# Optimization experiments

Measured on AMD Instinct MI355X. Metric: run time of the kernel, lower is better.

The kernel has to match this reference:

```python
import jax, jax.numpy as jnp
import numpy as np

NUM_GROUP, GROUP_SIZE = 128, 32
MASK = (64, 32, 32)
FEAT_DIM, N_POINTS = 1024, 2048
NBR_K = int(1.2 * GROUP_SIZE)  # int(nbr_ratio * group_size) = 38
SUPPORT, NBHD = 8, 32
W_RECON, W_MATCH, W_LATENT, W_MAN = 1.0, 1.0, 1.0, 0.1

gather = jax.vmap(lambda p, i: p[i])  # batched index_points

def sqdist(a, b):  # [B,M,3],[B,N,3] -> [B,M,N]
    return (jnp.sum(a * a, -1)[:, :, None] + jnp.sum(b * b, -1)[:, None, :]
            - 2.0 * jnp.einsum('bmd,bnd->bmn', a, b))

def knn_idx(q, db, k):  # indices into db of k nearest to each query
    return jax.lax.top_k(-sqdist(q, db), k)[1]

def fps(pts, G):  # farthest point sampling, [B,N,3] -> [B,G] indices
    b, n, _ = pts.shape
    def step(carry, _):
        min_d, far = carry
        cur = jnp.take_along_axis(pts, far[:, None, None], axis=1)
        min_d = jnp.minimum(min_d, jnp.sum((pts - cur) ** 2, -1))
        return (min_d, jnp.argmax(min_d, -1).astype(jnp.int32)), far
    init = (jnp.full((b, n), 1e10, dtype=pts.dtype), jnp.zeros((b,), jnp.int32))
    _, idxs = jax.lax.scan(step, init, None, length=G)
    return idxs.T

def bn(h, g, b_, m, v):  # BatchNorm1d, eval-mode running stats
    return (h - m) * jax.lax.rsqrt(v + 1e-5) * g + b_

def chamfer_l1(a, b):
    d = sqdist(a, b)
    d1 = jnp.sqrt(jnp.maximum(jnp.min(d, axis=2), 1e-12))
    d2 = jnp.sqrt(jnp.maximum(jnp.min(d, axis=1), 1e-12))
    return 0.5 * (d1.mean() + d2.mean())

def estimate_normals(xyz, K):  # PCA normal per point + direction disambiguation
    nb = gather(xyz, knn_idx(xyz, xyz, K))          # [B,N,K,3]
    c = nb - nb.mean(axis=2, keepdims=True)
    cov = jnp.einsum('bnki,bnkj->bnij', c, c) / K   # [B,N,3,3]
    _, v = jnp.linalg.eigh(cov)
    n = v[..., 0]                                   # smallest-eigenvalue eigvec
    proj = jnp.einsum('bnkd,bnd->bn', nb - xyz[:, :, None, :], n)
    return n * jnp.where(proj >= 0.0, 1.0, -1.0)[..., None]

def forward_all(pts, W1, b1, g1, be1, m1, v1, W2, b2, W3, b3, g2, be2, m2, v2,
                W4, b4, D1W, D1b, D2W, D2b, D3W, D3b, D4W, D4b):
    bsz = pts.shape[0]
    def encoder(x):  # PCN encoder: pointwise convs + global max pooling
        n = x.shape[1]
        h = jax.nn.relu(bn(x @ W1.T + b1, g1, be1, m1, v1))
        h = h @ W2.T + b2                           # [B,n,256]
        gmax = h.max(axis=1)
        h = jnp.concatenate([jnp.broadcast_to(gmax[:, None, :], (bsz, n, gmax.shape[-1])), h], axis=-1)
        h = jax.nn.relu(bn(h @ W3.T + b3, g2, be2, m2, v2))
        return (h @ W4.T + b4).max(axis=1)          # [B,FEAT_DIM]
    def decoder(z):
        h = jax.nn.relu(z @ D1W.T + D1b)
        h = jax.nn.relu(h @ D2W.T + D2b)
        h = jax.nn.relu(h @ D3W.T + D3b)
        return (h @ D4W.T + D4b).reshape(bsz, -1, 3)
    # --- Group divider: FPS centers + knn neighborhoods (centered) ---
    center = gather(pts, fps(pts, NUM_GROUP))       # [B,G,3]
    nbrs = gather(pts, knn_idx(center, pts, GROUP_SIZE)) - center[:, :, None, :]
    o1, o2 = MASK[0], MASK[0] + MASK[1]             # identity perm partition
    ng = (nbrs[:, :o1], nbrs[:, o1:o2], nbrs[:, o2:])
    cg = (center[:, :o1], center[:, o1:o2], center[:, o2:])
    rebuild0 = (ng[0] + cg[0][:, :, None, :]).reshape(bsz, -1, 3)
    feat = encoder(rebuild0)
    pred = decoder(feat)                            # [B,N_POINTS,3]
    # shape reconstruction loss
    idx = knn_idx(cg[0], pred, NBR_K)
    l_recon = W_RECON * chamfer_l1(rebuild0, gather(pred, idx).reshape(bsz, -1, 3))
    # shape matching loss
    rebuild1 = (ng[1] + cg[1][:, :, None, :]).reshape(bsz, -1, 3)
    idx = knn_idx(cg[1], pred, NBR_K)
    l_match = W_MATCH * chamfer_l1(rebuild1, gather(pred, idx).reshape(bsz, -1, 3))
    # latent reconstruction (detached input) - SmoothL1
    idx = knn_idx(cg[2], pred, GROUP_SIZE)
    feat_recon = encoder(jax.lax.stop_gradient(gather(pred, idx).reshape(bsz, -1, 3)))
    diff = feat - feat_recon
    ad = jnp.abs(diff)
    l_latent = W_LATENT * jnp.where(ad < 1.0, 0.5 * diff * diff, ad - 0.5).mean()
    # manifoldness (normal consistency) constraint
    normals = estimate_normals(pred, NBHD)
    nb = gather(normals, knn_idx(pred, pred, SUPPORT))  # [B,N,8,3]
    a = nb[:, :, :1, :]
    cos = jnp.sum(a * nb, -1) / (jnp.maximum(jnp.linalg.norm(a, axis=-1), 1e-6)
                                 * jnp.maximum(jnp.linalg.norm(nb, axis=-1), 1e-6))
    l_man = W_MAN * jnp.std(1.0 - cos, axis=-1, ddof=1).mean(axis=-1).mean()
    total = l_recon + l_match + l_latent + l_man
    return total, l_recon, l_match, l_latent, l_man


def setup_inputs() -> dict:
    ks = jax.random.split(jax.random.key(0), 10)
    rn = lambda k, sh: jax.random.normal(k, sh, jnp.float32) * 0.02
    z, o = jnp.zeros, jnp.ones
    return dict(
        pts=jax.random.normal(ks[0], (16, 2048, 3), jnp.float32),
        W1=rn(ks[1], (128, 3)), b1=z(128), g1=o(128), be1=z(128), m1=z(128), v1=o(128),
        W2=rn(ks[2], (256, 128)), b2=z(256),
        W3=rn(ks[3], (512, 512)), b3=z(512), g2=o(512), be2=z(512), m2=z(512), v2=o(512),
        W4=rn(ks[4], (FEAT_DIM, 512)), b4=z(FEAT_DIM),
        D1W=rn(ks[5], (2048, FEAT_DIM)), D1b=z(2048),
        D2W=rn(ks[6], (2048, 2048)), D2b=z(2048),
        D3W=rn(ks[7], (2048, 2048)), D3b=z(2048),
        D4W=rn(ks[8], (3 * N_POINTS, 2048)), D4b=z(3 * N_POINTS),
    )


def reference(pts, W1, b1, g1, be1, m1, v1, W2, b2, W3, b3, g2, be2, m2, v2,
              W4, b4, D1W, D1b, D2W, D2b, D3W, D3b, D4W, D4b):
    return forward_all(pts, W1, b1, g1, be1, m1, v1, W2, b2, W3, b3, g2, be2,
                       m2, v2, W4, b4, D1W, D1b, D2W, D2b, D3W, D3b, D4W, D4b)
```

## Files before the change

### kernel.cpp

```cpp
#include <hip/hip_runtime.h>
#include <math.h>

#define BSZ 16
#define NPTS 2048
#define NG 128
#define GS 32
#define NBRK 38

typedef _Float16 f16;
typedef _Float16 f16x8 __attribute__((ext_vector_type(8)));
typedef float f32x4 __attribute__((ext_vector_type(4)));

__device__ __forceinline__ unsigned fkey(float x) {
    unsigned u = __float_as_uint(x);
    return (u >> 31) ? ~u : (u | 0x80000000u);
}
__device__ __forceinline__ float fkey_inv(unsigned k) {
    unsigned u = (k >> 31) ? (k ^ 0x80000000u) : ~k;
    return __uint_as_float(u);
}

__device__ __forceinline__ unsigned wave_min_u32(unsigned v) {
    unsigned t;
    t = (unsigned)__builtin_amdgcn_update_dpp(-1, (int)v, 0x111, 0xF, 0xF, false);
    v = v < t ? v : t;
    t = (unsigned)__builtin_amdgcn_update_dpp(-1, (int)v, 0x112, 0xF, 0xF, false);
    v = v < t ? v : t;
    t = (unsigned)__builtin_amdgcn_update_dpp(-1, (int)v, 0x114, 0xF, 0xF, false);
    v = v < t ? v : t;
    t = (unsigned)__builtin_amdgcn_update_dpp(-1, (int)v, 0x118, 0xF, 0xF, false);
    v = v < t ? v : t;
    t = (unsigned)__builtin_amdgcn_update_dpp(-1, (int)v, 0x142, 0xA, 0xF, false);
    v = v < t ? v : t;
    t = (unsigned)__builtin_amdgcn_update_dpp(-1, (int)v, 0x143, 0xC, 0xF, false);
    v = v < t ? v : t;
    return (unsigned)__builtin_amdgcn_readlane((int)v, 63);
}

__device__ __forceinline__ unsigned long long wave_max_u64(unsigned long long v) {
#define DPPSTEP(ctrl, rmask)                                                                \
    {                                                                                       \
        unsigned tlo = (unsigned)__builtin_amdgcn_update_dpp(0, (int)(unsigned)v, ctrl,     \
                                                             rmask, 0xF, false);            \
        unsigned thi = (unsigned)__builtin_amdgcn_update_dpp(0, (int)(unsigned)(v >> 32),   \
                                                             ctrl, rmask, 0xF, false);      \
        unsigned long long t = ((unsigned long long)thi << 32) | tlo;                       \
        v = t > v ? t : v;                                                                  \
    }
    DPPSTEP(0x111, 0xF)
    DPPSTEP(0x112, 0xF)
    DPPSTEP(0x114, 0xF)
    DPPSTEP(0x118, 0xF)
    DPPSTEP(0x142, 0xA)
    DPPSTEP(0x143, 0xC)
#undef DPPSTEP
    unsigned rlo = (unsigned)__builtin_amdgcn_readlane((int)(unsigned)v, 63);
    unsigned rhi = (unsigned)__builtin_amdgcn_readlane((int)(unsigned)(v >> 32), 63);
    return ((unsigned long long)rhi << 32) | rlo;
}

__global__ __launch_bounds__(256, 1) void fps_kernel_v5(const float* __restrict__ pts,
                                                        float* __restrict__ center) {
    int b = blockIdx.x;
    const float* P = pts + (size_t)b * NPTS * 3;
    int tid = threadIdx.x;
    int lane = tid & 63, wave = tid >> 6;
    __shared__ __align__(16) float Pl[NPTS * 3];
    __shared__ __align__(16) float slot[2][4][8];
#pragma unroll
    for (int i = 0; i < 6; ++i) {
        int v4 = tid + i * 256;
        ((f32x4*)Pl)[v4] = ((const f32x4*)P)[v4];
    }
    __syncthreads();
    float px[8], py[8], pz[8], mind[8];
#pragma unroll
    for (int m = 0; m < 8; ++m) {
        int j = tid + (m << 8);
        px[m] = Pl[j * 3 + 0];
        py[m] = Pl[j * 3 + 1];
        pz[m] = Pl[j * 3 + 2];
        mind[m] = 1e10f;
    }
    float cx = Pl[0], cy = Pl[1], cz = Pl[2];
    float* C = center + (size_t)b * NG * 3;
#pragma unroll 1
    for (int g = 0; g < NG; ++g) {
        if (tid == 0) {
            C[g * 3 + 0] = cx; C[g * 3 + 1] = cy; C[g * 3 + 2] = cz;
        }
        if (g == NG - 1) break;
        float best0 = -1.f, best1 = -1.f;
        int bm0 = 0, bm1 = 1;
#pragma unroll
        for (int m = 0; m < 8; m += 2) {
            float dx0 = px[m] - cx, dy0 = py[m] - cy, dz0 = pz[m] - cz;
            float d0 = dx0 * dx0 + dy0 * dy0 + dz0 * dz0;
            float md0 = fminf(mind[m], d0);
            mind[m] = md0;
            if (md0 > best0) { best0 = md0; bm0 = m; }
            float dx1 = px[m + 1] - cx, dy1 = py[m + 1] - cy, dz1 = pz[m + 1] - cz;
            float d1 = dx1 * dx1 + dy1 * dy1 + dz1 * dz1;
            float md1 = fminf(mind[m + 1], d1);
            mind[m + 1] = md1;
            if (md1 > best1) { best1 = md1; bm1 = m + 1; }
        }
        bool t = (best1 > best0) || (best1 == best0 && bm1 < bm0);
        float bv = t ? best1 : best0;
        int bi = t ? bm1 : bm0;
        unsigned j = (unsigned)(tid + (bi << 8));
        unsigned long long key =
            ((unsigned long long)__float_as_uint(bv) << 32) | (unsigned)(~j);
        key = wave_max_u64(key);
        unsigned bj = ~(unsigned)key;
        int par = g & 1;
        if (lane < 3) slot[par][wave][2 + lane] = Pl[bj * 3 + lane];
        if (lane == 0) {
            slot[par][wave][0] = __uint_as_float((unsigned)key);
            slot[par][wave][1] = __uint_as_float((unsigned)(key >> 32));
        }
        __syncthreads();
        unsigned long long kb = 0ull;
        float nx = 0.f, ny = 0.f, nz = 0.f;
#pragma unroll
        for (int w = 0; w < 4; ++w) {
            f32x4 v = *(const f32x4*)&slot[par][w][0];
            float vz = slot[par][w][4];
            unsigned long long kk =
                ((unsigned long long)__float_as_uint(v[1]) << 32) | __float_as_uint(v[0]);
            bool tw = kk > kb;
            kb = tw ? kk : kb;
            nx = tw ? v[2] : nx;
            ny = tw ? v[3] : ny;
            nz = tw ? vz : nz;
        }
        cx = nx; cy = ny; cz = nz;
    }
}

__device__ __forceinline__ void knn_query(const float* __restrict__ q,
                                          const float* __restrict__ db,
                                          int k, int* __restrict__ o, int lane) {
    const unsigned KINF = 0xFFFFFFFFu;
    float qx = q[0], qy = q[1], qz = q[2];
    float qq = qx * qx + qy * qy + qz * qz;
    unsigned key[32];
    unsigned c0 = KINF, c1 = KINF, c2 = KINF, c3 = KINF;
#pragma unroll
    for (int m = 0; m < 32; ++m) {
        int j = lane + (m << 6);
        float bx = db[j * 3 + 0], by = db[j * 3 + 1], bz = db[j * 3 + 2];
        float dv = qq + bx * bx + by * by + bz * bz - 2.0f * (qx * bx + qy * by + qz * bz);
        unsigned qd = (unsigned)fminf(fmaxf(dv, 0.f) * 8192.0f, 2097151.f);
        unsigned kk = (qd << 11) | (unsigned)j;
        key[m] = kk;
        if (kk < c3) {
            if (kk < c2) {
                c3 = c2;
                if (kk < c1) {
                    c2 = c1;
                    if (kk < c0) { c1 = c0; c0 = kk; } else c1 = kk;
                } else c2 = kk;
            } else c3 = kk;
        }
    }
    unsigned hw = c3;
    int ncached = 4;
    for (int r = 0; r < k; ++r) {
        bool need = (c0 == KINF) && (ncached < 32);
        if (__any(need)) {
            unsigned best = KINF;
#pragma unroll
            for (int m = 0; m < 32; ++m) {
                unsigned v = key[m];
                best = (v > hw && v < best) ? v : best;
            }
            if (need) {
                c0 = best;
                hw = best;
                ncached = (best == KINF) ? 32 : ncached + 1;
            }
        }
        unsigned g = wave_min_u32(c0);
        if (lane == 0) o[r] = (int)(g & 0x7FFu);
        if (((g & 0x7FFu) & 63u) == (unsigned)lane) {
            c0 = c1; c1 = c2; c2 = c3; c3 = KINF;
        }
    }
}

__global__ void knn_kernel_v7(const float* __restrict__ Q, int q_bstride, int q_off, int nq,
                              const float* __restrict__ DB, int k,
                              int* __restrict__ out, int nbatch) {
    int wave = threadIdx.x >> 6, lane = threadIdx.x & 63;
    int qidx = blockIdx.x * 4 + wave;
    if (qidx >= nbatch * nq) return;
    int b = qidx / nq, qi = qidx % nq;
    knn_query(Q + ((size_t)b * q_bstride + q_off + qi) * 3,
              DB + (size_t)b * NPTS * 3, k, out + (size_t)qidx * k, lane);
}

__global__ void knn_post_kernel(const float* __restrict__ center,
                                const float* __restrict__ pred,
                                int* __restrict__ idxa, int* __restrict__ idxb,
                                int* __restrict__ idxc, int* __restrict__ knn32) {
    int wave = threadIdx.x >> 6, lane = threadIdx.x & 63;
    if (blockIdx.x < 512) {
        int qidx = blockIdx.x * 4 + wave;
        int b = qidx >> 7, qi = qidx & 127;
        const float* q = center + ((size_t)b * NG + qi) * 3;
        const float* db = pred + (size_t)b * NPTS * 3;
        int k; int* o;
        if (qi < 64) { k = NBRK; o = idxa + ((size_t)b * 64 + qi) * NBRK; }
        else if (qi < 96) { k = NBRK; o = idxb + ((size_t)b * 32 + qi - 64) * NBRK; }
        else { k = GS; o = idxc + ((size_t)b * 32 + qi - 96) * GS; }
        knn_query(q, db, k, o, lane);
    } else {
        int qidx = (blockIdx.x - 512) * 4 + wave;
        int b = qidx >> 11, qi = qidx & 2047;
        const float* db = pred + (size_t)b * NPTS * 3;
        knn_query(db + (size_t)qi * 3, db, GS, knn32 + (size_t)qidx * GS, lane);
    }
}

__global__ void gather_rebuild_kernel(const float* __restrict__ pts,
                                      const int* __restrict__ knnc,
                                      float* __restrict__ rebuild0,
                                      float* __restrict__ rebuild1,
                                      f32x4* __restrict__ r0p4,
                                      f32x4* __restrict__ r1p4) {
    int t = blockIdx.x * 256 + threadIdx.x;
    if (t < BSZ * 2048) {
        int b = t >> 11, j = t & 2047;
        int s = knnc[(size_t)b * (NG * GS) + j];
        const float* p = pts + ((size_t)b * NPTS + s) * 3;
        float x = p[0], y = p[1], z = p[2];
        rebuild0[(size_t)t * 3 + 0] = x;
        rebuild0[(size_t)t * 3 + 1] = y;
        rebuild0[(size_t)t * 3 + 2] = z;
        r0p4[t] = (f32x4){x, y, z, x * x + y * y + z * z};
    } else {
        int tt = t - BSZ * 2048;
        int b = tt >> 10, j = tt & 1023;
        int s = knnc[(size_t)b * (NG * GS) + 2048 + j];
        const float* p = pts + ((size_t)b * NPTS + s) * 3;
        float x = p[0], y = p[1], z = p[2];
        rebuild1[(size_t)tt * 3 + 0] = x;
        rebuild1[(size_t)tt * 3 + 1] = y;
        rebuild1[(size_t)tt * 3 + 2] = z;
        r1p4[tt] = (f32x4){x, y, z, x * x + y * y + z * z};
    }
}

__global__ void gather_abc_kernel(const float* __restrict__ pred,
                                  const int* __restrict__ idxa,
                                  const int* __restrict__ idxb,
                                  const int* __restrict__ idxc,
                                  f32x4* __restrict__ gap4,
                                  f32x4* __restrict__ gbp4,
                                  float* __restrict__ gathc) {
    const int NA = BSZ * 2432, NB_ = BSZ * 1216, NC = BSZ * 1024;
    int t = blockIdx.x * 256 + threadIdx.x;
    if (t < NA) {
        int b = t / 2432, j = t - b * 2432;
        int s = idxa[(size_t)b * 2432 + j];
        const float* p = pred + ((size_t)b * NPTS + s) * 3;
        float x = p[0], y = p[1], z = p[2];
        gap4[t] = (f32x4){x, y, z, x * x + y * y + z * z};
    } else if (t < NA + NB_) {
        int tt = t - NA;
        int b = tt / 1216, j = tt - b * 1216;
        int s = idxb[(size_t)b * 1216 + j];
        const float* p = pred + ((size_t)b * NPTS + s) * 3;
        float x = p[0], y = p[1], z = p[2];
        gbp4[tt] = (f32x4){x, y, z, x * x + y * y + z * z};
    } else if (t < NA + NB_ + NC) {
        int tt = t - NA - NB_;
        int b = tt >> 10, j = tt & 1023;
        int s = idxc[(size_t)b * 1024 + j];
        const float* p = pred + ((size_t)b * NPTS + s) * 3;
        gathc[(size_t)tt * 3 + 0] = p[0];
        gathc[(size_t)tt * 3 + 1] = p[1];
        gathc[(size_t)tt * 3 + 2] = p[2];
    }
}

__global__ void cvt_all_kernel(const float* __restrict__ W2, const float* __restrict__ W3,
                               const float* __restrict__ W4, f16* __restrict__ W2h,
                               f16* __restrict__ W3h, f16* __restrict__ W4h) {
    int t = blockIdx.x * 256 + threadIdx.x;
    if (t < 32768) {
        int n = t >> 7, k = t & 127;
        W2h[t] = (f16)W2[(size_t)n * 128 + k];
    } else if (t < 163840) {
        int u = t - 32768;
        int n = u >> 8, k = u & 255;
        W3h[u] = (f16)W3[(size_t)n * 512 + 256 + k];
    } else if (t < 688128) {
        int u = t - 163840;
        int n = u >> 9, k = u & 511;
        W4h[u] = (f16)W4[(size_t)n * 512 + k];
    }
}

__global__ void layer1_kernel(const float* __restrict__ X, const float* __restrict__ W1,
                              const float* __restrict__ b1, const float* __restrict__ g1,
                              const float* __restrict__ be1, const float* __restrict__ m1,
                              const float* __restrict__ v1, f16* __restrict__ H1, int M) {
    __shared__ float w[384], bb[128], sg[128], sb[128], sm[128], sv[128];
    for (int i = threadIdx.x; i < 384; i += 256) w[i] = W1[i];
    if (threadIdx.x < 128) {
        int c = threadIdx.x;
        bb[c] = b1[c]; sg[c] = g1[c]; sb[c] = be1[c]; sm[c] = m1[c]; sv[c] = v1[c];
    }
    __syncthreads();
    int t = blockIdx.x * 256 + threadIdx.x;
    if (t >= M * 16) return;
    int row = t >> 4, cg = (t & 15) * 8;
    float x0 = X[(size_t)row * 3], x1 = X[(size_t)row * 3 + 1], x2 = X[(size_t)row * 3 + 2];
    f16x8 outv;
#pragma unroll
    for (int j = 0; j < 8; ++j) {
        int c = cg + j;
        float tv = x0 * w[c * 3] + x1 * w[c * 3 + 1] + x2 * w[c * 3 + 2] + bb[c];
        float vv = (tv - sm[c]) * rsqrtf(sv[c] + 1e-5f) * sg[c] + sb[c];
        outv[j] = (f16)fmaxf(vv, 0.f);
    }
    *(f16x8*)&H1[(size_t)row * 128 + cg] = outv;
}

__global__ __launch_bounds__(256) void mfma_gemm_kernel(
        const f16* __restrict__ A, const f16* __restrict__ W, int K, int N,
        const float* __restrict__ bias, const float* __restrict__ bias2d,
        const float* __restrict__ bng, const float* __restrict__ bnb,
        const float* __restrict__ bnm, const float* __restrict__ bnv,
        f16* __restrict__ Cout, unsigned* __restrict__ maxkey,
        int rows_per_batch, int relu) {
    __shared__ f16 Als[128 * 40];
    __shared__ f16 Bls[128 * 40];
    int tid = threadIdx.x;
    int lane = tid & 63;
    int wave = tid >> 6;
    int wm = wave & 1, wn = wave >> 1;
    int c16 = lane & 15, quad = lane >> 4;
    int gx = gridDim.x;
    int nwg = gx * gridDim.y;
    int lin = blockIdx.y * gx + blockIdx.x;
    int qc = nwg >> 3, rc = nwg & 7;
    int xcd = lin & 7, pos = lin >> 3;
    int nlin = (xcd < rc ? xcd * (qc + 1) : rc * (qc + 1) + (xcd - rc) * qc) + pos;
    int row0 = (nlin / gx) * 128, col0 = (nlin % gx) * 128;
    int sr = tid >> 2;
    int skc = (tid & 3) * 8;

    f32x4 acc[4][4];
#pragma unroll
    for (int i = 0; i < 4; ++i)
#pragma unroll
        for (int j = 0; j < 4; ++j) acc[i][j] = (f32x4){0.f, 0.f, 0.f, 0.f};

    const f16* Ab = A + (size_t)(row0 + sr) * K + skc;
    const f16* Ab2 = A + (size_t)(row0 + sr + 64) * K + skc;
    const f16* Wb = W + (size_t)(col0 + sr) * K + skc;
    const f16* Wb2 = W + (size_t)(col0 + sr + 64) * K + skc;

    f16x8 pa0 = *(const f16x8*)Ab;
    f16x8 pa1 = *(const f16x8*)Ab2;
    f16x8 pb0 = *(const f16x8*)Wb;
    f16x8 pb1 = *(const f16x8*)Wb2;

    for (int k0 = 0; k0 < K; k0 += 32) {
        *(f16x8*)&Als[sr * 40 + skc] = pa0;
        *(f16x8*)&Als[(sr + 64) * 40 + skc] = pa1;
        *(f16x8*)&Bls[sr * 40 + skc] = pb0;
        *(f16x8*)&Bls[(sr + 64) * 40 + skc] = pb1;
        __syncthreads();
        if (k0 + 32 < K) {
            int kn = k0 + 32;
            pa0 = *(const f16x8*)(Ab + kn);
            pa1 = *(const f16x8*)(Ab2 + kn);
            pb0 = *(const f16x8*)(Wb + kn);
            pb1 = *(const f16x8*)(Wb2 + kn);
        }
        f16x8 af[4], bf[4];
#pragma unroll
        for (int s = 0; s < 4; ++s) {
            af[s] = *(const f16x8*)&Als[(wm * 64 + s * 16 + c16) * 40 + quad * 8];
            bf[s] = *(const f16x8*)&Bls[(wn * 64 + s * 16 + c16) * 40 + quad * 8];
        }
#pragma unroll
        for (int ms = 0; ms < 4; ++ms)
#pragma unroll
            for (int ns = 0; ns < 4; ++ns)
                acc[ms][ns] = __builtin_amdgcn_mfma_f32_16x16x32_f16(af[ms], bf[ns],
                                                                     acc[ms][ns], 0, 0, 0);
        __syncthreads();
    }

    int b = row0 / rows_per_batch;
#pragma unroll
    for (int ns = 0; ns < 4; ++ns) {
        int col = col0 + wn * 64 + ns * 16 + c16;
        float bv = bias ? bias[col] : 0.f;
        float b2v = bias2d ? bias2d[(size_t)b * N + col] : 0.f;
        float mx = -3e38f;
#pragma unroll
        for (int ms = 0; ms < 4; ++ms) {
#pragma unroll
            for (int j = 0; j < 4; ++j) {
                float v = acc[ms][ns][j] + bv + b2v;
                if (bng) v = (v - bnm[col]) * rsqrtf(bnv[col] + 1e-5f) * bng[col] + bnb[col];
                if (relu) v = fmaxf(v, 0.f);
                if (Cout)
                    Cout[(size_t)(row0 + wm * 64 + ms * 16 + quad * 4 + j) * N + col] = (f16)v;
                mx = fmaxf(mx, v);
            }
        }
        if (maxkey) {
            mx = fmaxf(mx, __shfl_xor(mx, 16, 64));
            mx = fmaxf(mx, __shfl_xor(mx, 32, 64));
            if (quad == 0) atomicMax(&maxkey[(size_t)b * N + col], fkey(mx));
        }
    }
}

__global__ void skinny_v2_kernel(const float* __restrict__ A, const float* __restrict__ W,
                                 int ldw, int woff, const float* __restrict__ bias,
                                 float* __restrict__ C, int K, int N, int relu, int akey) {
    int wave = threadIdx.x >> 6, lane = threadIdx.x & 63;
    int col = blockIdx.x * 4 + wave;
    if (col >= N) return;
    const float* w = W + (size_t)col * ldw + woff;
    float acc[16];
#pragma unroll
    for (int m = 0; m < 16; ++m) acc[m] = 0.f;
    for (int k0 = 0; k0 < K; k0 += 256) {
        f32x4 wv = *(const f32x4*)(w + k0 + lane * 4);
#pragma unroll
        for (int m = 0; m < 16; ++m) {
            f32x4 av = *(const f32x4*)(A + (size_t)m * K + k0 + lane * 4);
            if (akey) {
#pragma unroll
                for (int u = 0; u < 4; ++u) av[u] = fkey_inv(__float_as_uint(av[u]));
            }
            acc[m] += av[0] * wv[0] + av[1] * wv[1] + av[2] * wv[2] + av[3] * wv[3];
        }
    }
#pragma unroll
    for (int m = 0; m < 16; ++m)
#pragma unroll
        for (int s = 1; s < 64; s <<= 1) acc[m] += __shfl_xor(acc[m], s, 64);
    if (lane == 0) {
        float bv = bias[col];
#pragma unroll
        for (int m = 0; m < 16; ++m) {
            float v = acc[m] + bv;
            if (relu) v = fmaxf(v, 0.f);
            C[(size_t)m * N + col] = v;
        }
    }
}

__global__ __launch_bounds__(256) void chamfer4_kernel(const f32x4* __restrict__ r0p4,
                                                       const f32x4* __restrict__ gap4,
                                                       const f32x4* __restrict__ r1p4,
                                                       const f32x4* __restrict__ gbp4,
                                                       float* __restrict__ accum) {
    __shared__ __align__(16) float Bl[2432 * 4];
    int blk = blockIdx.x;
    const f32x4 *A4, *B4; int na, nb, base, bpb; float* slot;
    if (blk < 128)      { A4 = r0p4; na = 2048; B4 = gap4; nb = 2432; slot = accum + 0; base = 0;   bpb = 8; }
    else if (blk < 288) { A4 = gap4; na = 2432; B4 = r0p4; nb = 2048; slot = accum + 1; base = 128; bpb = 10; }
    else if (blk < 352) { A4 = r1p4; na = 1024; B4 = gbp4; nb = 1216; slot = accum + 2; base = 288; bpb = 4; }
    else                { A4 = gbp4; na = 1216; B4 = r1p4; nb = 1024; slot = accum + 3; base = 352; bpb = 5; }
    int rel = blk - base;
    int b = rel / bpb, chunk = rel - b * bpb;
    for (int i = threadIdx.x; i < nb; i += 256)
        ((f32x4*)Bl)[i] = B4[(size_t)b * nb + i];
    __syncthreads();
    int aidx = chunk * 256 + threadIdx.x;
    float val = 0.f;
    if (aidx < na) {
        f32x4 a = A4[(size_t)b * na + aidx];
        float m2x = -2.f * a[0], m2y = -2.f * a[1], m2z = -2.f * a[2];
        float m0 = 3e38f, m1 = 3e38f, m2 = 3e38f, m3 = 3e38f;
        for (int j = 0; j < nb; j += 4) {
            f32x4 b0 = ((const f32x4*)Bl)[j + 0];
            f32x4 b1 = ((const f32x4*)Bl)[j + 1];
            f32x4 b2 = ((const f32x4*)Bl)[j + 2];
            f32x4 b3 = ((const f32x4*)Bl)[j + 3];
            float t0 = fmaf(m2z, b0[2], fmaf(m2y, b0[1], fmaf(m2x, b0[0], b0[3])));
            float t1 = fmaf(m2z, b1[2], fmaf(m2y, b1[1], fmaf(m2x, b1[0], b1[3])));
            float t2 = fmaf(m2z, b2[2], fmaf(m2y, b2[1], fmaf(m2x, b2[0], b2[3])));
            float t3 = fmaf(m2z, b3[2], fmaf(m2y, b3[1], fmaf(m2x, b3[0], b3[3])));
            m0 = fminf(m0, t0); m1 = fminf(m1, t1);
            m2 = fminf(m2, t2); m3 = fminf(m3, t3);
        }
        float m = fminf(fminf(m0, m1), fminf(m2, m3));
        val = sqrtf(fmaxf(a[3] + m, 1e-12f));
    }
    __shared__ float sdata[256];
    sdata[threadIdx.x] = val;
    __syncthreads();
    for (int s = 128; s > 0; s >>= 1) {
        if (threadIdx.x < s) sdata[threadIdx.x] += sdata[threadIdx.x + s];
        __syncthreads();
    }
    if (threadIdx.x == 0) atomicAdd(slot, sdata[0]);
}

__global__ void latent_kernel(const unsigned* __restrict__ k1,
                              const unsigned* __restrict__ k2,
                              int n, float* __restrict__ slot) {
    int t = blockIdx.x * blockDim.x + threadIdx.x;
    float val = 0.f;
    if (t < n) {
        float d = fkey_inv(k1[t]) - fkey_inv(k2[t]);
        float ad = fabsf(d);
        val = (ad < 1.f) ? (0.5f * d * d) : (ad - 0.5f);
    }
    __shared__ float sdata[256];
    sdata[threadIdx.x] = val;
    __syncthreads();
    for (int s = 128; s > 0; s >>= 1) {
        if (threadIdx.x < s) sdata[threadIdx.x] += sdata[threadIdx.x + s];
        __syncthreads();
    }
    if (threadIdx.x == 0) atomicAdd(slot, sdata[0]);
}

__device__ void smallest_evec(double cxx, double cxy, double cxz,
                              double cyy, double cyz, double czz, double ev[3]) {
    double p1 = cxy * cxy + cxz * cxz + cyz * cyz;
    double q = (cxx + cyy + czz) / 3.0;
    double p2 = (cxx - q) * (cxx - q) + (cyy - q) * (cyy - q) + (czz - q) * (czz - q) + 2.0 * p1;
    double lam = q;
    if (p2 > 0.0) {
        double p = sqrt(p2 / 6.0);
        double b00 = (cxx - q) / p, b11 = (cyy - q) / p, b22 = (czz - q) / p;
        double b01 = cxy / p, b02 = cxz / p, b12 = cyz / p;
        double detB = b00 * (b11 * b22 - b12 * b12) - b01 * (b01 * b22 - b12 * b02)
                    + b02 * (b01 * b12 - b11 * b02);
        double r = detB * 0.5;
        r = r < -1.0 ? -1.0 : (r > 1.0 ? 1.0 : r);
        double phi = acos(r) / 3.0;
        lam = q + 2.0 * p * cos(phi + 2.0943951023931953);
    }
    double r0x = cxx - lam, r0y = cxy, r0z = cxz;
    double r1x = cxy, r1y = cyy - lam, r1z = cyz;
    double r2x = cxz, r2y = cyz, r2z = czz - lam;
    double c0x = r0y * r1z - r0z * r1y, c0y = r0z * r1x - r0x * r1z, c0z = r0x * r1y - r0y * r1x;
    double c1x = r0y * r2z - r0z * r2y, c1y = r0z * r2x - r0x * r2z, c1z = r0x * r2y - r0y * r2x;
    double c2x = r1y * r2z - r1z * r2y, c2y = r1z * r2x - r1x * r2z, c2z = r1x * r2y - r1y * r2x;
    double n0 = c0x * c0x + c0y * c0y + c0z * c0z;
    double n1 = c1x * c1x + c1y * c1y + c1z * c1z;
    double n2 = c2x * c2x + c2y * c2y + c2z * c2z;
    double bx = c0x, by = c0y, bz = c0z, bn = n0;
    if (n1 > bn) { bx = c1x; by = c1y; bz = c1z; bn = n1; }
    if (n2 > bn) { bx = c2x; by = c2y; bz = c2z; bn = n2; }
    if (bn < 1e-280) { ev[0] = 1.0; ev[1] = 0.0; ev[2] = 0.0; return; }
    double inv = 1.0 / sqrt(bn);
    ev[0] = bx * inv; ev[1] = by * inv; ev[2] = bz * inv;
}

__global__ __launch_bounds__(64) void normals_kernel(const float* __restrict__ pred,
                                                     const int* __restrict__ knn,
                                                     float* __restrict__ nrm) {
    int t = blockIdx.x * 64 + threadIdx.x;
    if (t >= BSZ * NPTS) return;
    int b = t / NPTS, i = t % NPTS;
    const float* P = pred + (size_t)b * NPTS * 3;
    const int* id = knn + (size_t)t * 32;
    double sx = 0, sy = 0, sz = 0;
    double sxx = 0, sxy = 0, sxz = 0, syy = 0, syz = 0, szz = 0;
#pragma unroll
    for (int k0 = 0; k0 < 32; k0 += 4) {
        int4 jj = *(const int4*)&id[k0];
#pragma unroll
        for (int u = 0; u < 4; ++u) {
            int j = (u == 0) ? jj.x : (u == 1) ? jj.y : (u == 2) ? jj.z : jj.w;
            double x = (double)P[j * 3 + 0];
            double y = (double)P[j * 3 + 1];
            double z = (double)P[j * 3 + 2];
            sx += x; sy += y; sz += z;
            sxx += x * x; sxy += x * y; sxz += x * z;
            syy += y * y; syz += y * z; szz += z * z;
        }
    }
    double mx = sx * (1.0 / 32.0), my = sy * (1.0 / 32.0), mz = sz * (1.0 / 32.0);
    double cxx = sxx * (1.0 / 32.0) - mx * mx;
    double cxy = sxy * (1.0 / 32.0) - mx * my;
    double cxz = sxz * (1.0 / 32.0) - mx * mz;
    double cyy = syy * (1.0 / 32.0) - my * my;
    double cyz = syz * (1.0 / 32.0) - my * mz;
    double czz = szz * (1.0 / 32.0) - mz * mz;
    double ev[3];
    smallest_evec(cxx, cxy, cxz, cyy, cyz, czz, ev);
    float qx = P[i * 3 + 0], qy = P[i * 3 + 1], qz = P[i * 3 + 2];
    double proj = (sx - 32.0 * (double)qx) * ev[0] + (sy - 32.0 * (double)qy) * ev[1]
                + (sz - 32.0 * (double)qz) * ev[2];
    double s = (proj >= 0.0) ? 1.0 : -1.0;
    nrm[(size_t)t * 3 + 0] = (float)(ev[0] * s);
    nrm[(size_t)t * 3 + 1] = (float)(ev[1] * s);
    nrm[(size_t)t * 3 + 2] = (float)(ev[2] * s);
}

__global__ void manifold_kernel(const float* __restrict__ nrm, const int* __restrict__ knn,
                                int kstride, float* __restrict__ slot) {
    int t = blockIdx.x * blockDim.x + threadIdx.x;
    float val = 0.f;
    if (t < BSZ * NPTS) {
        int b = t / NPTS;
        const float* NB = nrm + (size_t)b * NPTS * 3;
        const int* id = knn + (size_t)t * kstride;
        int j0 = id[0];
        float ax = NB[j0 * 3 + 0], ay = NB[j0 * 3 + 1], az = NB[j0 * 3 + 2];
        float an = fmaxf(sqrtf(ax * ax + ay * ay + az * az), 1e-6f);
        float x[8]; float s = 0.f;
        for (int k = 0; k < 8; ++k) {
            int j = id[k];
            float bx = NB[j * 3 + 0], by = NB[j * 3 + 1], bz = NB[j * 3 + 2];
            float bn_ = fmaxf(sqrtf(bx * bx + by * by + bz * bz), 1e-6f);
            float c = (ax * bx + ay * by + az * bz) / (an * bn_);
            x[k] = 1.f - c; s += x[k];
        }
        float mean = s / 8.f;
        float var = 0.f;
        for (int k = 0; k < 8; ++k) { float d = x[k] - mean; var += d * d; }
        val = sqrtf(var / 7.f);
    }
    __shared__ float sdata[256];
    sdata[threadIdx.x] = val;
    __syncthreads();
    for (int s2 = 128; s2 > 0; s2 >>= 1) {
        if (threadIdx.x < s2) sdata[threadIdx.x] += sdata[threadIdx.x + s2];
        __syncthreads();
    }
    if (threadIdx.x == 0) atomicAdd(slot, sdata[0]);
}

__global__ void finalize_kernel(const float* __restrict__ acc, float* __restrict__ out) {
    float l_recon = 0.5f * (acc[0] / (16.f * 2048.f) + acc[1] / (16.f * 2432.f));
    float l_match = 0.5f * (acc[2] / (16.f * 1024.f) + acc[3] / (16.f * 1216.f));
    float l_latent = acc[4] / (16.f * 1024.f);
    float l_man = 0.1f * (acc[5] / (16.f * 2048.f));
    out[0] = l_recon + l_match + l_latent + l_man;
    out[1] = l_recon;
    out[2] = l_match;
    out[3] = l_latent;
    out[4] = l_man;
}

extern "C" void kernel_launch(void* const* d_in, const int* in_sizes, int n_in,
                              void* d_out, int out_size, void* d_ws, size_t ws_size,
                              hipStream_t stream) {
    (void)in_sizes; (void)n_in; (void)out_size; (void)ws_size;
    const float* pts = (const float*)d_in[0];
    const float* W1 = (const float*)d_in[1];
    const float* b1 = (const float*)d_in[2];
    const float* g1 = (const float*)d_in[3];
    const float* be1 = (const float*)d_in[4];
    const float* m1 = (const float*)d_in[5];
    const float* v1 = (const float*)d_in[6];
    const float* W2 = (const float*)d_in[7];
    const float* b2 = (const float*)d_in[8];
    const float* W3 = (const float*)d_in[9];
    const float* b3 = (const float*)d_in[10];
    const float* g2 = (const float*)d_in[11];
    const float* be2 = (const float*)d_in[12];
    const float* m2 = (const float*)d_in[13];
    const float* v2 = (const float*)d_in[14];
    const float* W4 = (const float*)d_in[15];
    const float* b4 = (const float*)d_in[16];
    const float* D1W = (const float*)d_in[17];
    const float* D1b = (const float*)d_in[18];
    const float* D2W = (const float*)d_in[19];
    const float* D2b = (const float*)d_in[20];
    const float* D3W = (const float*)d_in[21];
    const float* D3b = (const float*)d_in[22];
    const float* D4W = (const float*)d_in[23];
    const float* D4b = (const float*)d_in[24];

    char* ws = (char*)d_ws;
    size_t off = 0;
    auto alloc = [&](size_t bytes) -> void* {
        void* p = ws + off;
        off += (bytes + 255) & ~(size_t)255;
        return p;
    };
    float* center   = (float*)alloc((size_t)BSZ * NG * 3 * 4);
    int*   knnc     = (int*)  alloc((size_t)BSZ * NG * GS * 4);
    float* rebuild0 = (float*)alloc((size_t)BSZ * 2048 * 3 * 4);
    float* rebuild1 = (float*)alloc((size_t)BSZ * 1024 * 3 * 4);
    f32x4* r0p4     = (f32x4*)alloc((size_t)BSZ * 2048 * 16);
    f32x4* r1p4     = (f32x4*)alloc((size_t)BSZ * 1024 * 16);
    f16*   W2h      = (f16*)  alloc((size_t)256 * 128 * 2);
    f16*   W3h      = (f16*)  alloc((size_t)512 * 256 * 2);
    f16*   W4h      = (f16*)  alloc((size_t)1024 * 512 * 2);
    f16*   H1h      = (f16*)  alloc((size_t)BSZ * 2048 * 128 * 2);
    f16*   H2h      = (f16*)  alloc((size_t)BSZ * 2048 * 256 * 2);
    f16*   H3h      = (f16*)  alloc((size_t)BSZ * 2048 * 512 * 2);
    unsigned* keybase = (unsigned*)alloc(((size_t)BSZ * 2560 + 64) * 4);
    unsigned* gmaxkey1 = keybase;
    unsigned* gmaxkey2 = keybase + (size_t)BSZ * 256;
    unsigned* featkey1 = keybase + (size_t)BSZ * 512;
    unsigned* featkey2 = keybase + (size_t)BSZ * 512 + (size_t)BSZ * 1024;
    float* accum = (float*)(keybase + (size_t)BSZ * 2560);
    float* gpart    = (float*)alloc((size_t)BSZ * 512 * 4);
    float* dh1      = (float*)alloc((size_t)BSZ * 2048 * 4);
    float* dh2      = (float*)alloc((size_t)BSZ * 2048 * 4);
    float* dh3      = (float*)alloc((size_t)BSZ * 2048 * 4);
    float* pred     = (float*)alloc((size_t)BSZ * 6144 * 4);
    int*   idxa     = (int*)  alloc((size_t)BSZ * 64 * NBRK * 4);
    int*   idxb     = (int*)  alloc((size_t)BSZ * 32 * NBRK * 4);
    int*   idxc     = (int*)  alloc((size_t)BSZ * 32 * 32 * 4);
    f32x4* gap4     = (f32x4*)alloc((size_t)BSZ * 2432 * 16);
    f32x4* gbp4     = (f32x4*)alloc((size_t)BSZ * 1216 * 16);
    float* gathc    = (float*)alloc((size_t)BSZ * 1024 * 3 * 4);
    int*   knn32    = (int*)  alloc((size_t)BSZ * 2048 * 32 * 4);
    float* nrmbuf   = (float*)alloc((size_t)BSZ * 2048 * 3 * 4);

    hipMemsetAsync(keybase, 0, ((size_t)BSZ * 2560 + 8) * 4, stream);

    cvt_all_kernel<<<2688, 256, 0, stream>>>(W2, W3, W4, W2h, W3h, W4h);

    fps_kernel_v5<<<BSZ, 256, 0, stream>>>(pts, center);
    knn_kernel_v7<<<(BSZ * NG + 3) / 4, 256, 0, stream>>>(center, NG, 0, NG, pts, GS,
                                                          knnc, BSZ);
    gather_rebuild_kernel<<<(BSZ * 3072) / 256, 256, 0, stream>>>(pts, knnc, rebuild0,
                                                                  rebuild1, r0p4, r1p4);

    auto enc = [&](const float* X, int n, unsigned* gkey, unsigned* fkeyout) {
        int M = BSZ * n;
        layer1_kernel<<<M / 16, 256, 0, stream>>>(X, W1, b1, g1, be1, m1, v1, H1h, M);
        mfma_gemm_kernel<<<dim3(256 / 128, M / 128), 256, 0, stream>>>(
            H1h, W2h, 128, 256, b2, nullptr, nullptr, nullptr, nullptr, nullptr,
            H2h, gkey, n, 0);
        skinny_v2_kernel<<<(512 + 3) / 4, 256, 0, stream>>>(
            (const float*)gkey, W3, 512, 0, b3, gpart, 256, 512, 0, 1);
        mfma_gemm_kernel<<<dim3(512 / 128, M / 128), 256, 0, stream>>>(
            H2h, W3h, 256, 512, nullptr, gpart, g2, be2, m2, v2, H3h, nullptr, n, 1);
        mfma_gemm_kernel<<<dim3(1024 / 128, M / 128), 256, 0, stream>>>(
            H3h, W4h, 512, 1024, b4, nullptr, nullptr, nullptr, nullptr, nullptr,
            nullptr, fkeyout, n, 0);
    };

    enc(rebuild0, 2048, gmaxkey1, featkey1);

    skinny_v2_kernel<<<2048 / 4, 256, 0, stream>>>((const float*)featkey1, D1W, 1024, 0,
                                                   D1b, dh1, 1024, 2048, 1, 1);
    skinny_v2_kernel<<<2048 / 4, 256, 0, stream>>>(dh1, D2W, 2048, 0, D2b, dh2,
                                                   2048, 2048, 1, 0);
    skinny_v2_kernel<<<2048 / 4, 256, 0, stream>>>(dh2, D3W, 2048, 0, D3b, dh3,
                                                   2048, 2048, 1, 0);
    skinny_v2_kernel<<<6144 / 4, 256, 0, stream>>>(dh3, D4W, 2048, 0, D4b, pred,
                                                   2048, 6144, 0, 0);

    knn_post_kernel<<<512 + (BSZ * NPTS) / 4, 256, 0, stream>>>(center, pred, idxa,
                                                                idxb, idxc, knn32);
    gather_abc_kernel<<<(BSZ * 4672) / 256, 256, 0, stream>>>(pred, idxa, idxb, idxc,
                                                              gap4, gbp4, gathc);
    chamfer4_kernel<<<432, 256, 0, stream>>>(r0p4, gap4, r1p4, gbp4, accum);
    normals_kernel<<<(BSZ * NPTS) / 64, 64, 0, stream>>>(pred, knn32, nrmbuf);

    enc(gathc, 1024, gmaxkey2, featkey2);
    latent_kernel<<<(BSZ * 1024 + 255) / 256, 256, 0, stream>>>(featkey1, featkey2,
                                                                BSZ * 1024, accum + 4);
    manifold_kernel<<<(BSZ * 2048 + 255) / 256, 256, 0, stream>>>(nrmbuf, knn32, 32,
                                                                  accum + 5);

    finalize_kernel<<<1, 1, 0, stream>>>(accum, (float*)d_out);
}
```

Before: 665.1 us.

## Pack point clouds as float4 with squared norm and merge loss tail kernels

```diff
diff --git a/kernel.cpp b/kernel.cpp
--- a/kernel.cpp
+++ b/kernel.cpp
@@ -60,7 +60,7 @@
 }
 
 __global__ __launch_bounds__(256, 1) void fps_kernel_v5(const float* __restrict__ pts,
-                                                        float* __restrict__ center) {
+                                                        f32x4* __restrict__ center4) {
     int b = blockIdx.x;
     const float* P = pts + (size_t)b * NPTS * 3;
     int tid = threadIdx.x;
@@ -83,12 +83,10 @@
         mind[m] = 1e10f;
     }
     float cx = Pl[0], cy = Pl[1], cz = Pl[2];
-    float* C = center + (size_t)b * NG * 3;
+    f32x4* C4 = center4 + (size_t)b * NG;
 #pragma unroll 1
     for (int g = 0; g < NG; ++g) {
-        if (tid == 0) {
-            C[g * 3 + 0] = cx; C[g * 3 + 1] = cy; C[g * 3 + 2] = cz;
-        }
+        if (tid == 0) C4[g] = (f32x4){cx, cy, cz, cx * cx + cy * cy + cz * cz};
         if (g == NG - 1) break;
         float best0 = -1.f, best1 = -1.f;
         int bm0 = 0, bm1 = 1;
@@ -138,19 +136,20 @@
     }
 }
 
-__device__ __forceinline__ void knn_query(const float* __restrict__ q,
-                                          const float* __restrict__ db,
-                                          int k, int* __restrict__ o, int lane) {
+__device__ __forceinline__ void knn_query_p4(f32x4 q, const f32x4* __restrict__ db4,
+                                             int k, int* __restrict__ o, int lane) {
     const unsigned KINF = 0xFFFFFFFFu;
-    float qx = q[0], qy = q[1], qz = q[2];
-    float qq = qx * qx + qy * qy + qz * qz;
+    float m2x = -2.f * q[0], m2y = -2.f * q[1], m2z = -2.f * q[2], qq = q[3];
     unsigned key[32];
     unsigned c0 = KINF, c1 = KINF, c2 = KINF, c3 = KINF;
 #pragma unroll
     for (int m = 0; m < 32; ++m) {
         int j = lane + (m << 6);
-        float bx = db[j * 3 + 0], by = db[j * 3 + 1], bz = db[j * 3 + 2];
-        float dv = qq + bx * bx + by * by + bz * bz - 2.0f * (qx * bx + qy * by + qz * bz);
+        f32x4 b = db4[j];
+        float t = fmaf(m2x, b[0], b[3]);
+        t = fmaf(m2y, b[1], t);
+        t = fmaf(m2z, b[2], t);
+        float dv = qq + t;
         unsigned qd = (unsigned)fminf(fmaxf(dv, 0.f) * 8192.0f, 2097151.f);
         unsigned kk = (qd << 11) | (unsigned)j;
         key[m] = kk;
@@ -189,105 +188,85 @@
     }
 }
 
-__global__ void knn_kernel_v7(const float* __restrict__ Q, int q_bstride, int q_off, int nq,
-                              const float* __restrict__ DB, int k,
-                              int* __restrict__ out, int nbatch) {
+__global__ void knn_group_kernel(const f32x4* __restrict__ center4,
+                                 const f32x4* __restrict__ pts4,
+                                 int* __restrict__ knnc) {
     int wave = threadIdx.x >> 6, lane = threadIdx.x & 63;
     int qidx = blockIdx.x * 4 + wave;
-    if (qidx >= nbatch * nq) return;
-    int b = qidx / nq, qi = qidx % nq;
-    knn_query(Q + ((size_t)b * q_bstride + q_off + qi) * 3,
-              DB + (size_t)b * NPTS * 3, k, out + (size_t)qidx * k, lane);
-}
-
-__global__ void knn_post_kernel(const float* __restrict__ center,
-                                const float* __restrict__ pred,
+    int b = qidx >> 7, qi = qidx & 127;
+    knn_query_p4(center4[(size_t)b * NG + qi], pts4 + (size_t)b * NPTS, GS,
+                 knnc + (size_t)qidx * GS, lane);
+}
+
+__global__ void knn_post_kernel(const f32x4* __restrict__ center4,
+                                const f32x4* __restrict__ pred4,
                                 int* __restrict__ idxa, int* __restrict__ idxb,
                                 int* __restrict__ idxc, int* __restrict__ knn32) {
     int wave = threadIdx.x >> 6, lane = threadIdx.x & 63;
     if (blockIdx.x < 512) {
         int qidx = blockIdx.x * 4 + wave;
         int b = qidx >> 7, qi = qidx & 127;
-        const float* q = center + ((size_t)b * NG + qi) * 3;
-        const float* db = pred + (size_t)b * NPTS * 3;
+        const f32x4* db4 = pred4 + (size_t)b * NPTS;
         int k; int* o;
         if (qi < 64) { k = NBRK; o = idxa + ((size_t)b * 64 + qi) * NBRK; }
         else if (qi < 96) { k = NBRK; o = idxb + ((size_t)b * 32 + qi - 64) * NBRK; }
         else { k = GS; o = idxc + ((size_t)b * 32 + qi - 96) * GS; }
-        knn_query(q, db, k, o, lane);
+        knn_query_p4(center4[(size_t)b * NG + qi], db4, k, o, lane);
     } else {
         int qidx = (blockIdx.x - 512) * 4 + wave;
         int b = qidx >> 11, qi = qidx & 2047;
-        const float* db = pred + (size_t)b * NPTS * 3;
-        knn_query(db + (size_t)qi * 3, db, GS, knn32 + (size_t)qidx * GS, lane);
-    }
-}
-
-__global__ void gather_rebuild_kernel(const float* __restrict__ pts,
+        const f32x4* db4 = pred4 + (size_t)b * NPTS;
+        knn_query_p4(db4[qi], db4, GS, knn32 + (size_t)qidx * GS, lane);
+    }
+}
+
+__global__ void gather_rebuild_kernel(const f32x4* __restrict__ pts4,
                                       const int* __restrict__ knnc,
-                                      float* __restrict__ rebuild0,
-                                      float* __restrict__ rebuild1,
                                       f32x4* __restrict__ r0p4,
                                       f32x4* __restrict__ r1p4) {
     int t = blockIdx.x * 256 + threadIdx.x;
     if (t < BSZ * 2048) {
         int b = t >> 11, j = t & 2047;
         int s = knnc[(size_t)b * (NG * GS) + j];
-        const float* p = pts + ((size_t)b * NPTS + s) * 3;
-        float x = p[0], y = p[1], z = p[2];
-        rebuild0[(size_t)t * 3 + 0] = x;
-        rebuild0[(size_t)t * 3 + 1] = y;
-        rebuild0[(size_t)t * 3 + 2] = z;
-        r0p4[t] = (f32x4){x, y, z, x * x + y * y + z * z};
+        r0p4[t] = pts4[(size_t)b * NPTS + s];
     } else {
         int tt = t - BSZ * 2048;
         int b = tt >> 10, j = tt & 1023;
         int s = knnc[(size_t)b * (NG * GS) + 2048 + j];
-        const float* p = pts + ((size_t)b * NPTS + s) * 3;
-        float x = p[0], y = p[1], z = p[2];
-        rebuild1[(size_t)tt * 3 + 0] = x;
-        rebuild1[(size_t)tt * 3 + 1] = y;
-        rebuild1[(size_t)tt * 3 + 2] = z;
-        r1p4[tt] = (f32x4){x, y, z, x * x + y * y + z * z};
-    }
-}
-
-__global__ void gather_abc_kernel(const float* __restrict__ pred,
+        r1p4[tt] = pts4[(size_t)b * NPTS + s];
+    }
+}
+
+__global__ void gather_abc_kernel(const f32x4* __restrict__ pred4,
                                   const int* __restrict__ idxa,
                                   const int* __restrict__ idxb,
                                   const int* __restrict__ idxc,
                                   f32x4* __restrict__ gap4,
                                   f32x4* __restrict__ gbp4,
-                                  float* __restrict__ gathc) {
+                                  f32x4* __restrict__ gathc4) {
     const int NA = BSZ * 2432, NB_ = BSZ * 1216, NC = BSZ * 1024;
     int t = blockIdx.x * 256 + threadIdx.x;
     if (t < NA) {
         int b = t / 2432, j = t - b * 2432;
         int s = idxa[(size_t)b * 2432 + j];
-        const float* p = pred + ((size_t)b * NPTS + s) * 3;
-        float x = p[0], y = p[1], z = p[2];
-        gap4[t] = (f32x4){x, y, z, x * x + y * y + z * z};
+        gap4[t] = pred4[(size_t)b * NPTS + s];
     } else if (t < NA + NB_) {
         int tt = t - NA;
         int b = tt / 1216, j = tt - b * 1216;
         int s = idxb[(size_t)b * 1216 + j];
-        const float* p = pred + ((size_t)b * NPTS + s) * 3;
-        float x = p[0], y = p[1], z = p[2];
-        gbp4[tt] = (f32x4){x, y, z, x * x + y * y + z * z};
+        gbp4[tt] = pred4[(size_t)b * NPTS + s];
     } else if (t < NA + NB_ + NC) {
         int tt = t - NA - NB_;
         int b = tt >> 10, j = tt & 1023;
         int s = idxc[(size_t)b * 1024 + j];
-        const float* p = pred + ((size_t)b * NPTS + s) * 3;
-        gathc[(size_t)tt * 3 + 0] = p[0];
-        gathc[(size_t)tt * 3 + 1] = p[1];
-        gathc[(size_t)tt * 3 + 2] = p[2];
+        gathc4[tt] = pred4[(size_t)b * NPTS + s];
     }
 }
 
 __global__ void cvt_all_kernel(const float* __restrict__ W2, const float* __restrict__ W3,
-                               const float* __restrict__ W4, f16* __restrict__ W2h,
-                               f16* __restrict__ W3h, f16* __restrict__ W4h) {
+                               const float* __restrict__ W4, const float* __restrict__ pts,
+                               f16* __restrict__ W2h, f16* __restrict__ W3h,
+                               f16* __restrict__ W4h, f32x4* __restrict__ pts4) {
     int t = blockIdx.x * 256 + threadIdx.x;
     if (t < 32768) {
         int n = t >> 7, k = t & 127;
@@ -300,10 +279,24 @@
         int u = t - 163840;
         int n = u >> 9, k = u & 511;
         W4h[u] = (f16)W4[(size_t)n * 512 + k];
-    }
-}
-
-__global__ void layer1_kernel(const float* __restrict__ X, const float* __restrict__ W1,
+    } else if (t < 688128 + BSZ * NPTS) {
+        int u = t - 688128;
+        float x = pts[(size_t)u * 3 + 0], y = pts[(size_t)u * 3 + 1],
+              z = pts[(size_t)u * 3 + 2];
+        pts4[u] = (f32x4){x, y, z, x * x + y * y + z * z};
+    }
+}
+
+__global__ void pack_pred4_kernel(const float* __restrict__ pred,
+                                  f32x4* __restrict__ pred4) {
+    int t = blockIdx.x * 256 + threadIdx.x;
+    if (t >= BSZ * NPTS) return;
+    float x = pred[(size_t)t * 3 + 0], y = pred[(size_t)t * 3 + 1],
+          z = pred[(size_t)t * 3 + 2];
+    pred4[t] = (f32x4){x, y, z, x * x + y * y + z * z};
+}
+
+__global__ void layer1_kernel(const f32x4* __restrict__ X4, const float* __restrict__ W1,
                               const float* __restrict__ b1, const float* __restrict__ g1,
                               const float* __restrict__ be1, const float* __restrict__ m1,
                               const float* __restrict__ v1, f16* __restrict__ H1, int M) {
@@ -317,7 +310,8 @@
     int t = blockIdx.x * 256 + threadIdx.x;
     if (t >= M * 16) return;
     int row = t >> 4, cg = (t & 15) * 8;
-    float x0 = X[(size_t)row * 3], x1 = X[(size_t)row * 3 + 1], x2 = X[(size_t)row * 3 + 2];
+    f32x4 xv = X4[row];
+    float x0 = xv[0], x1 = xv[1], x2 = xv[2];
     f16x8 outv;
 #pragma unroll
     for (int j = 0; j < 8; ++j) {
@@ -509,26 +503,6 @@
     if (threadIdx.x == 0) atomicAdd(slot, sdata[0]);
 }
 
-__global__ void latent_kernel(const unsigned* __restrict__ k1,
-                              const unsigned* __restrict__ k2,
-                              int n, float* __restrict__ slot) {
-    int t = blockIdx.x * blockDim.x + threadIdx.x;
-    float val = 0.f;
-    if (t < n) {
-        float d = fkey_inv(k1[t]) - fkey_inv(k2[t]);
-        float ad = fabsf(d);
-        val = (ad < 1.f) ? (0.5f * d * d) : (ad - 0.5f);
-    }
-    __shared__ float sdata[256];
-    sdata[threadIdx.x] = val;
-    __syncthreads();
-    for (int s = 128; s > 0; s >>= 1) {
-        if (threadIdx.x < s) sdata[threadIdx.x] += sdata[threadIdx.x + s];
-        __syncthreads();
-    }
-    if (threadIdx.x == 0) atomicAdd(slot, sdata[0]);
-}
-
 __device__ void smallest_evec(double cxx, double cxy, double cxz,
                               double cyy, double cyz, double czz, double ev[3]) {
     double p1 = cxy * cxy + cxz * cxz + cyz * cyz;
@@ -563,13 +537,13 @@
     ev[0] = bx * inv; ev[1] = by * inv; ev[2] = bz * inv;
 }
 
-__global__ __launch_bounds__(64) void normals_kernel(const float* __restrict__ pred,
+__global__ __launch_bounds__(64) void normals_kernel(const f32x4* __restrict__ pred4,
                                                      const int* __restrict__ knn,
                                                      float* __restrict__ nrm) {
     int t = blockIdx.x * 64 + threadIdx.x;
     if (t >= BSZ * NPTS) return;
     int b = t / NPTS, i = t % NPTS;
-    const float* P = pred + (size_t)b * NPTS * 3;
+    const f32x4* P4 = pred4 + (size_t)b * NPTS;
     const int* id = knn + (size_t)t * 32;
     double sx = 0, sy = 0, sz = 0;
     double sxx = 0, sxy = 0, sxz = 0, syy = 0, syz = 0, szz = 0;
@@ -579,9 +553,8 @@
 #pragma unroll
         for (int u = 0; u < 4; ++u) {
             int j = (u == 0) ? jj.x : (u == 1) ? jj.y : (u == 2) ? jj.z : jj.w;
-            double x = (double)P[j * 3 + 0];
-            double y = (double)P[j * 3 + 1];
-            double z = (double)P[j * 3 + 2];
+            f32x4 p = P4[j];
+            double x = (double)p[0], y = (double)p[1], z = (double)p[2];
             sx += x; sy += y; sz += z;
             sxx += x * x; sxy += x * y; sxz += x * z;
             syy += y * y; syz += y * z; szz += z * z;
@@ -596,23 +569,28 @@
     double czz = szz * (1.0 / 32.0) - mz * mz;
     double ev[3];
     smallest_evec(cxx, cxy, cxz, cyy, cyz, czz, ev);
-    float qx = P[i * 3 + 0], qy = P[i * 3 + 1], qz = P[i * 3 + 2];
-    double proj = (sx - 32.0 * (double)qx) * ev[0] + (sy - 32.0 * (double)qy) * ev[1]
-                + (sz - 32.0 * (double)qz) * ev[2];
+    f32x4 q = P4[i];
+    double proj = (sx - 32.0 * (double)q[0]) * ev[0] + (sy - 32.0 * (double)q[1]) * ev[1]
+                + (sz - 32.0 * (double)q[2]) * ev[2];
     double s = (proj >= 0.0) ? 1.0 : -1.0;
     nrm[(size_t)t * 3 + 0] = (float)(ev[0] * s);
     nrm[(size_t)t * 3 + 1] = (float)(ev[1] * s);
     nrm[(size_t)t * 3 + 2] = (float)(ev[2] * s);
 }
 
-__global__ void manifold_kernel(const float* __restrict__ nrm, const int* __restrict__ knn,
-                                int kstride, float* __restrict__ slot) {
-    int t = blockIdx.x * blockDim.x + threadIdx.x;
+__global__ void loss_tail_kernel(const float* __restrict__ nrm,
+                                 const int* __restrict__ knn32,
+                                 const unsigned* __restrict__ k1,
+                                 const unsigned* __restrict__ k2,
+                                 float* __restrict__ accum) {
     float val = 0.f;
-    if (t < BSZ * NPTS) {
-        int b = t / NPTS;
+    float* slot;
+    if (blockIdx.x < 128) {
+        slot = accum + 5;
+        int t = blockIdx.x * 256 + threadIdx.x;
+        int b = t >> 11;
         const float* NB = nrm + (size_t)b * NPTS * 3;
-        const int* id = knn + (size_t)t * kstride;
+        const int* id = knn32 + (size_t)t * 32;
         int j0 = id[0];
         float ax = NB[j0 * 3 + 0], ay = NB[j0 * 3 + 1], az = NB[j0 * 3 + 2];
         float an = fmaxf(sqrtf(ax * ax + ay * ay + az * az), 1e-6f);
@@ -628,6 +606,12 @@
         float var = 0.f;
         for (int k = 0; k < 8; ++k) { float d = x[k] - mean; var += d * d; }
         val = sqrtf(var / 7.f);
+    } else {
+        slot = accum + 4;
+        int t = (blockIdx.x - 128) * 256 + threadIdx.x;
+        float d = fkey_inv(k1[t]) - fkey_inv(k2[t]);
+        float ad = fabsf(d);
+        val = (ad < 1.f) ? (0.5f * d * d) : (ad - 0.5f);
     }
     __shared__ float sdata[256];
     sdata[threadIdx.x] = val;
@@ -688,10 +672,10 @@
         off += (bytes + 255) & ~(size_t)255;
         return p;
     };
-    float* center   = (float*)alloc((size_t)BSZ * NG * 3 * 4);
+    f32x4* center4  = (f32x4*)alloc((size_t)BSZ * NG * 16);
+    f32x4* pts4     = (f32x4*)alloc((size_t)BSZ * NPTS * 16);
+    f32x4* pred4    = (f32x4*)alloc((size_t)BSZ * NPTS * 16);
     int*   knnc     = (int*)  alloc((size_t)BSZ * NG * GS * 4);
-    float* rebuild0 = (float*)alloc((size_t)BSZ * 2048 * 3 * 4);
-    float* rebuild1 = (float*)alloc((size_t)BSZ * 1024 * 3 * 4);
     f32x4* r0p4     = (f32x4*)alloc((size_t)BSZ * 2048 * 16);
     f32x4* r1p4     = (f32x4*)alloc((size_t)BSZ * 1024 * 16);
     f16*   W2h      = (f16*)  alloc((size_t)256 * 128 * 2);
@@ -716,23 +700,21 @@
     int*   idxc     = (int*)  alloc((size_t)BSZ * 32 * 32 * 4);
     f32x4* gap4     = (f32x4*)alloc((size_t)BSZ * 2432 * 16);
     f32x4* gbp4     = (f32x4*)alloc((size_t)BSZ * 1216 * 16);
-    float* gathc    = (float*)alloc((size_t)BSZ * 1024 * 3 * 4);
+    f32x4* gathc4   = (f32x4*)alloc((size_t)BSZ * 1024 * 16);
     int*   knn32    = (int*)  alloc((size_t)BSZ * 2048 * 32 * 4);
     float* nrmbuf   = (float*)alloc((size_t)BSZ * 2048 * 3 * 4);
 
     hipMemsetAsync(keybase, 0, ((size_t)BSZ * 2560 + 8) * 4, stream);
 
-    cvt_all_kernel<<<2688, 256, 0, stream>>>(W2, W3, W4, W2h, W3h, W4h);
-
-    fps_kernel_v5<<<BSZ, 256, 0, stream>>>(pts, center);
-    knn_kernel_v7<<<(BSZ * NG + 3) / 4, 256, 0, stream>>>(center, NG, 0, NG, pts, GS,
-                                                          knnc, BSZ);
-    gather_rebuild_kernel<<<(BSZ * 3072) / 256, 256, 0, stream>>>(pts, knnc, rebuild0,
-                                                                  rebuild1, r0p4, r1p4);
-
-    auto enc = [&](const float* X, int n, unsigned* gkey, unsigned* fkeyout) {
+    cvt_all_kernel<<<2816, 256, 0, stream>>>(W2, W3, W4, pts, W2h, W3h, W4h, pts4);
+
+    fps_kernel_v5<<<BSZ, 256, 0, stream>>>(pts, center4);
+    knn_group_kernel<<<(BSZ * NG) / 4, 256, 0, stream>>>(center4, pts4, knnc);
+    gather_rebuild_kernel<<<(BSZ * 3072) / 256, 256, 0, stream>>>(pts4, knnc, r0p4, r1p4);
+
+    auto enc = [&](const f32x4* X4, int n, unsigned* gkey, unsigned* fkeyout) {
         int M = BSZ * n;
-        layer1_kernel<<<M / 16, 256, 0, stream>>>(X, W1, b1, g1, be1, m1, v1, H1h, M);
+        layer1_kernel<<<M / 16, 256, 0, stream>>>(X4, W1, b1, g1, be1, m1, v1, H1h, M);
         mfma_gemm_kernel<<<dim3(256 / 128, M / 128), 256, 0, stream>>>(
             H1h, W2h, 128, 256, b2, nullptr, nullptr, nullptr, nullptr, nullptr,
             H2h, gkey, n, 0);
@@ -745,7 +727,7 @@
             nullptr, fkeyout, n, 0);
     };
 
-    enc(rebuild0, 2048, gmaxkey1, featkey1);
+    enc(r0p4, 2048, gmaxkey1, featkey1);
 
     skinny_v2_kernel<<<2048 / 4, 256, 0, stream>>>((const float*)featkey1, D1W, 1024, 0,
                                                    D1b, dh1, 1024, 2048, 1, 1);
@@ -755,19 +737,17 @@
                                                    2048, 2048, 1, 0);
     skinny_v2_kernel<<<6144 / 4, 256, 0, stream>>>(dh3, D4W, 2048, 0, D4b, pred,
                                                    2048, 6144, 0, 0);
-
-    knn_post_kernel<<<512 + (BSZ * NPTS) / 4, 256, 0, stream>>>(center, pred, idxa,
+    pack_pred4_kernel<<<(BSZ * NPTS) / 256, 256, 0, stream>>>(pred, pred4);
+
+    knn_post_kernel<<<512 + (BSZ * NPTS) / 4, 256, 0, stream>>>(center4, pred4, idxa,
                                                                 idxb, idxc, knn32);
-    gather_abc_kernel<<<(BSZ * 4672) / 256, 256, 0, stream>>>(pred, idxa, idxb, idxc,
-                                                              gap4, gbp4, gathc);
+    gather_abc_kernel<<<(BSZ * 4672) / 256, 256, 0, stream>>>(pred4, idxa, idxb, idxc,
+                                                              gap4, gbp4, gathc4);
     chamfer4_kernel<<<432, 256, 0, stream>>>(r0p4, gap4, r1p4, gbp4, accum);
-    normals_kernel<<<(BSZ * NPTS) / 64, 64, 0, stream>>>(pred, knn32, nrmbuf);
-
-    enc(gathc, 1024, gmaxkey2, featkey2);
-    latent_kernel<<<(BSZ * 1024 + 255) / 256, 256, 0, stream>>>(featkey1, featkey2,
-                                                                BSZ * 1024, accum + 4);
-    manifold_kernel<<<(BSZ * 2048 + 255) / 256, 256, 0, stream>>>(nrmbuf, knn32, 32,
-                                                                  accum + 5);
+    normals_kernel<<<(BSZ * NPTS) / 64, 64, 0, stream>>>(pred4, knn32, nrmbuf);
+
+    enc(gathc4, 1024, gmaxkey2, featkey2);
+    loss_tail_kernel<<<192, 256, 0, stream>>>(nrmbuf, knn32, featkey1, featkey2, accum);
 
     finalize_kernel<<<1, 1, 0, stream>>>(accum, (float*)d_out);
 }
```

Measured after the change: 668.8 us. No clear change (+0.6%).
